# Optimization experiments

Measured on AMD Instinct MI355X. Metric: run time of the kernel, lower is better.

Reference implementation:

```python
import jax, jax.numpy as jnp
import numpy as np

N = 1_500_000
CB, CT, CO, B = 96, 128, 96, 8
BN_EPS = 1e-5


def setup_inputs() -> dict:
    key = jax.random.key(0)
    k1, k2, k3, k4 = jax.random.split(key, 4)
    return {
        "backbone_F": jax.random.normal(k1, (N, CB), dtype=jnp.float32),
        "batch_idx": jax.random.randint(k2, (N,), 0, B, dtype=jnp.int32),
        "text_feats": jax.random.normal(k3, (B, CT), dtype=jnp.float32),
        "W": jax.random.normal(k4, (CB + CT, CO), dtype=jnp.float32) * (1.0 / np.sqrt(CB + CT)),
        "gamma": jnp.ones((CO,), dtype=jnp.float32),
        "beta": jnp.zeros((CO,), dtype=jnp.float32),
    }


def reference(backbone_F, batch_idx, text_feats, W, gamma, beta):
    # gather text feats per point via batch index: [N, CT]
    rep_text = text_feats[batch_idx]
    # concat backbone + text feats: [N, CB+CT]
    combined = jnp.concatenate([backbone_F, rep_text], axis=1)
    # 1x1 sparse conv == pointwise GEMM (no bias): [N, CO]
    x = combined @ W
    # BatchNorm (training mode: batch stats over the N points)
    mean = jnp.mean(x, axis=0)
    var = jnp.var(x, axis=0)
    x = (x - mean) * jax.lax.rsqrt(var + BN_EPS) * gamma + beta
    # ReLU
    return jnp.maximum(x, 0.0)
```

## Files before the change

kernel.cpp:

```cpp
#include <hip/hip_runtime.h>
#include <hip/hip_bf16.h>

#define N_PTS 1500000
#define CBCH 96
#define CTCH 128
#define COCH 96
#define NB 8
#define BN_EPS 1e-5f

#define GSUM_OFF 0
#define GSQ_OFF 96
#define SCALE_OFF 192
#define BIAS_OFF 288
#define T_OFF 384

typedef __attribute__((ext_vector_type(8))) short bf16x8;
typedef __attribute__((ext_vector_type(4))) float f32x4;

__device__ __forceinline__ unsigned short f2bf_rne(float f) {
    union { float f; unsigned u; } v; v.f = f;
    unsigned u = v.u;
    return (unsigned short)((u + 0x7FFFu + ((u >> 16) & 1u)) >> 16);
}

__global__ void k0_init(const float* __restrict__ text, const float* __restrict__ W,
                        float* __restrict__ ws) {
    if (blockIdx.x == NB) {
        for (int i = threadIdx.x; i < 192; i += blockDim.x) ws[i] = 0.f;
        return;
    }
    int b = blockIdx.x;
    int c = threadIdx.x;
    if (c < COCH) {
        float acc = 0.f;
        #pragma unroll 8
        for (int k = 0; k < CTCH; ++k)
            acc += text[b * CTCH + k] * W[(CBCH + k) * COCH + c];
        ws[T_OFF + b * COCH + c] = acc;
    }
}

__global__ void k2_finalize(const float* __restrict__ gamma, const float* __restrict__ beta,
                            float* __restrict__ ws) {
    int c = threadIdx.x;
    if (c < COCH) {
        float mean = ws[GSUM_OFF + c] * (1.f / (float)N_PTS);
        float var  = ws[GSQ_OFF + c] * (1.f / (float)N_PTS) - mean * mean;
        float scl  = gamma[c] * rsqrtf(var + BN_EPS);
        ws[SCALE_OFF + c] = scl;
        ws[BIAS_OFF + c]  = beta[c] - mean * scl;
    }
}


__device__ __forceinline__ void load_bfrag(const float* __restrict__ W, int grp, int lr,
                                           bf16x8 bf[6][3]) {
    #pragma unroll
    for (int ct = 0; ct < 6; ++ct)
        #pragma unroll
        for (int kt = 0; kt < 3; ++kt)
            #pragma unroll
            for (int j = 0; j < 8; ++j)
                bf[ct][kt][j] = (short)f2bf_rne(W[(kt * 32 + grp * 8 + j) * COCH + ct * 16 + lr]);
}

__device__ __forceinline__ void tile_gemm(const float* __restrict__ bb,
                                          const int* __restrict__ bidx,
                                          const float* __restrict__ sT,
                                          int base, int grp, int lr,
                                          const bf16x8 bf[6][3], f32x4 acc[6]) {
    #pragma unroll
    for (int r = 0; r < 4; ++r) {
        int b = bidx[base + grp * 4 + r];
        #pragma unroll
        for (int ct = 0; ct < 6; ++ct)
            acc[ct][r] = sT[b * COCH + ct * 16 + lr];
    }
    bf16x8 af[3];
    #pragma unroll
    for (int kt = 0; kt < 3; ++kt) {
        const float4* p = reinterpret_cast<const float4*>(bb + (size_t)(base + lr) * CBCH + kt * 32 + grp * 8);
        float4 x0 = p[0], x1 = p[1];
        af[kt][0] = (short)f2bf_rne(x0.x); af[kt][1] = (short)f2bf_rne(x0.y);
        af[kt][2] = (short)f2bf_rne(x0.z); af[kt][3] = (short)f2bf_rne(x0.w);
        af[kt][4] = (short)f2bf_rne(x1.x); af[kt][5] = (short)f2bf_rne(x1.y);
        af[kt][6] = (short)f2bf_rne(x1.z); af[kt][7] = (short)f2bf_rne(x1.w);
    }
    #pragma unroll
    for (int ct = 0; ct < 6; ++ct)
        #pragma unroll
        for (int kt = 0; kt < 3; ++kt)
            acc[ct] = __builtin_amdgcn_mfma_f32_16x16x32_bf16(af[kt], bf[ct][kt], acc[ct], 0, 0, 0);
}

__global__ __launch_bounds__(256, 2) void k1_stats(const float* __restrict__ bb,
                                                   const int* __restrict__ bidx,
                                                   const float* __restrict__ W,
                                                   float* __restrict__ ws) {
    __shared__ float sT[NB * COCH];
    __shared__ float sred[2][4][COCH];
    for (int i = threadIdx.x; i < NB * COCH; i += blockDim.x) sT[i] = ws[T_OFF + i];
    __syncthreads();

    const int lane = threadIdx.x & 63;
    const int wv = threadIdx.x >> 6;
    const int grp = lane >> 4, lr = lane & 15;

    bf16x8 bf[6][3];
    load_bfrag(W, grp, lr, bf);

    float sum[6] = {0.f, 0.f, 0.f, 0.f, 0.f, 0.f};
    float sq[6] = {0.f, 0.f, 0.f, 0.f, 0.f, 0.f};

    const int gw = blockIdx.x * 4 + wv;
    const int nw = gridDim.x * 4;
    const int NT = N_PTS / 16;
    for (int t = gw; t < NT; t += nw) {
        int base = t * 16;
        f32x4 acc[6];
        tile_gemm(bb, bidx, sT, base, grp, lr, bf, acc);
        #pragma unroll
        for (int ct = 0; ct < 6; ++ct)
            #pragma unroll
            for (int r = 0; r < 4; ++r) {
                float x = acc[ct][r];
                sum[ct] += x;
                sq[ct] += x * x;
            }
    }

    #pragma unroll
    for (int ct = 0; ct < 6; ++ct) {
        float s = sum[ct], q = sq[ct];
        s += __shfl_xor(s, 16); q += __shfl_xor(q, 16);
        s += __shfl_xor(s, 32); q += __shfl_xor(q, 32);
        if (lane < 16) {
            sred[0][wv][ct * 16 + lane] = s;
            sred[1][wv][ct * 16 + lane] = q;
        }
    }
    __syncthreads();
    if (threadIdx.x < COCH) {
        int c = threadIdx.x;
        float s = sred[0][0][c] + sred[0][1][c] + sred[0][2][c] + sred[0][3][c];
        float q = sred[1][0][c] + sred[1][1][c] + sred[1][2][c] + sred[1][3][c];
        atomicAdd(&ws[GSUM_OFF + c], s);
        atomicAdd(&ws[GSQ_OFF + c], q);
    }
}

__global__ __launch_bounds__(256, 2) void k3_out(const float* __restrict__ bb,
                                                 const int* __restrict__ bidx,
                                                 const float* __restrict__ W,
                                                 const float* __restrict__ ws,
                                                 float* __restrict__ out) {
    __shared__ float sT[NB * COCH];
    for (int i = threadIdx.x; i < NB * COCH; i += blockDim.x) sT[i] = ws[T_OFF + i];
    __syncthreads();

    const int lane = threadIdx.x & 63;
    const int wv = threadIdx.x >> 6;
    const int grp = lane >> 4, lr = lane & 15;

    bf16x8 bf[6][3];
    load_bfrag(W, grp, lr, bf);

    float sc[6], bs[6];
    #pragma unroll
    for (int ct = 0; ct < 6; ++ct) {
        sc[ct] = ws[SCALE_OFF + ct * 16 + lr];
        bs[ct] = ws[BIAS_OFF + ct * 16 + lr];
    }

    const int gw = blockIdx.x * 4 + wv;
    const int nw = gridDim.x * 4;
    const int NT = N_PTS / 16;
    for (int t = gw; t < NT; t += nw) {
        int base = t * 16;
        f32x4 acc[6];
        tile_gemm(bb, bidx, sT, base, grp, lr, bf, acc);
        #pragma unroll
        for (int ct = 0; ct < 6; ++ct)
            #pragma unroll
            for (int r = 0; r < 4; ++r) {
                float y = fmaxf(acc[ct][r] * sc[ct] + bs[ct], 0.f);
                out[(size_t)(base + grp * 4 + r) * COCH + ct * 16 + lr] = y;
            }
    }
}

extern "C" void kernel_launch(void* const* d_in, const int* in_sizes, int n_in,
                              void* d_out, int out_size, void* d_ws, size_t ws_size,
                              hipStream_t stream) {
    const float* bb    = (const float*)d_in[0];
    const int*   bidx  = (const int*)d_in[1];
    const float* text  = (const float*)d_in[2];
    const float* W     = (const float*)d_in[3];
    const float* gamma = (const float*)d_in[4];
    const float* beta  = (const float*)d_in[5];
    float* out = (float*)d_out;
    float* ws  = (float*)d_ws;

    hipLaunchKernelGGL(k0_init, dim3(NB + 1), dim3(128), 0, stream, text, W, ws);
    hipLaunchKernelGGL(k1_stats, dim3(2048), dim3(256), 0, stream, bb, bidx, W, ws);
    hipLaunchKernelGGL(k2_finalize, dim3(1), dim3(128), 0, stream, gamma, beta, ws);
    hipLaunchKernelGGL(k3_out, dim3(2048), dim3(256), 0, stream, bb, bidx, W, ws, out);
}
```

Before: 377.3 us.

## Transpose output MFMA for vectorized stores, fold finalize into output kernel, reverse traversal

Swaps the MFMA operand order in the output kernel so that each lane holds four consecutive channels of one point. This lets results go out as 16-byte nontemporal vector stores instead of scattered scalar stores. The BN finalize kernel is removed and its scale/bias computation moves into the output kernel's prologue via shared memory, saving one launch. The output kernel also walks tiles in reverse order to reuse the backbone data the stats pass left in L2/cache, and loads it with nontemporal hints.

```diff
diff --git a/kernel.cpp b/kernel.cpp
--- a/kernel.cpp
+++ b/kernel.cpp
@@ -10,8 +10,6 @@
 
 #define GSUM_OFF 0
 #define GSQ_OFF 96
-#define SCALE_OFF 192
-#define BIAS_OFF 288
 #define T_OFF 384
 
 typedef __attribute__((ext_vector_type(8))) short bf16x8;
@@ -40,18 +38,6 @@
     }
 }
 
-__global__ void k2_finalize(const float* __restrict__ gamma, const float* __restrict__ beta,
-                            float* __restrict__ ws) {
-    int c = threadIdx.x;
-    if (c < COCH) {
-        float mean = ws[GSUM_OFF + c] * (1.f / (float)N_PTS);
-        float var  = ws[GSQ_OFF + c] * (1.f / (float)N_PTS) - mean * mean;
-        float scl  = gamma[c] * rsqrtf(var + BN_EPS);
-        ws[SCALE_OFF + c] = scl;
-        ws[BIAS_OFF + c]  = beta[c] - mean * scl;
-    }
-}
-
 
 __device__ __forceinline__ void load_bfrag(const float* __restrict__ W, int grp, int lr,
                                            bf16x8 bf[6][3]) {
@@ -62,35 +48,6 @@
             #pragma unroll
             for (int j = 0; j < 8; ++j)
                 bf[ct][kt][j] = (short)f2bf_rne(W[(kt * 32 + grp * 8 + j) * COCH + ct * 16 + lr]);
-}
-
-__device__ __forceinline__ void tile_gemm(const float* __restrict__ bb,
-                                          const int* __restrict__ bidx,
-                                          const float* __restrict__ sT,
-                                          int base, int grp, int lr,
-                                          const bf16x8 bf[6][3], f32x4 acc[6]) {
-    #pragma unroll
-    for (int r = 0; r < 4; ++r) {
-        int b = bidx[base + grp * 4 + r];
-        #pragma unroll
-        for (int ct = 0; ct < 6; ++ct)
-            acc[ct][r] = sT[b * COCH + ct * 16 + lr];
-    }
-    bf16x8 af[3];
-    #pragma unroll
-    for (int kt = 0; kt < 3; ++kt) {
-        const float4* p = reinterpret_cast<const float4*>(bb + (size_t)(base + lr) * CBCH + kt * 32 + grp * 8);
-        float4 x0 = p[0], x1 = p[1];
-        af[kt][0] = (short)f2bf_rne(x0.x); af[kt][1] = (short)f2bf_rne(x0.y);
-        af[kt][2] = (short)f2bf_rne(x0.z); af[kt][3] = (short)f2bf_rne(x0.w);
-        af[kt][4] = (short)f2bf_rne(x1.x); af[kt][5] = (short)f2bf_rne(x1.y);
-        af[kt][6] = (short)f2bf_rne(x1.z); af[kt][7] = (short)f2bf_rne(x1.w);
-    }
-    #pragma unroll
-    for (int ct = 0; ct < 6; ++ct)
-        #pragma unroll
-        for (int kt = 0; kt < 3; ++kt)
-            acc[ct] = __builtin_amdgcn_mfma_f32_16x16x32_bf16(af[kt], bf[ct][kt], acc[ct], 0, 0, 0);
 }
 
 __global__ __launch_bounds__(256, 2) void k1_stats(const float* __restrict__ bb,
@@ -118,7 +75,29 @@
     for (int t = gw; t < NT; t += nw) {
         int base = t * 16;
         f32x4 acc[6];
-        tile_gemm(bb, bidx, sT, base, grp, lr, bf, acc);
+        #pragma unroll
+        for (int r = 0; r < 4; ++r) {
+            int b = bidx[base + grp * 4 + r];
+            #pragma unroll
+            for (int ct = 0; ct < 6; ++ct)
+                acc[ct][r] = sT[b * COCH + ct * 16 + lr];
+        }
+        bf16x8 af[3];
+        #pragma unroll
+        for (int kt = 0; kt < 3; ++kt) {
+            const f32x4* p = reinterpret_cast<const f32x4*>(bb + (size_t)(base + lr) * CBCH + kt * 32 + grp * 8);
+            f32x4 x0 = p[0], x1 = p[1];
+            #pragma unroll
+            for (int j = 0; j < 4; ++j) {
+                af[kt][j]     = (short)f2bf_rne(x0[j]);
+                af[kt][4 + j] = (short)f2bf_rne(x1[j]);
+            }
+        }
+        #pragma unroll
+        for (int ct = 0; ct < 6; ++ct)
+            #pragma unroll
+            for (int kt = 0; kt < 3; ++kt)
+                acc[ct] = __builtin_amdgcn_mfma_f32_16x16x32_bf16(af[kt], bf[ct][kt], acc[ct], 0, 0, 0);
         #pragma unroll
         for (int ct = 0; ct < 6; ++ct)
             #pragma unroll
@@ -152,10 +131,22 @@
 __global__ __launch_bounds__(256, 2) void k3_out(const float* __restrict__ bb,
                                                  const int* __restrict__ bidx,
                                                  const float* __restrict__ W,
+                                                 const float* __restrict__ gamma,
+                                                 const float* __restrict__ beta,
                                                  const float* __restrict__ ws,
                                                  float* __restrict__ out) {
     __shared__ float sT[NB * COCH];
+    __shared__ float sScale[COCH];
+    __shared__ float sBias[COCH];
     for (int i = threadIdx.x; i < NB * COCH; i += blockDim.x) sT[i] = ws[T_OFF + i];
+    if (threadIdx.x < COCH) {
+        int c = threadIdx.x;
+        float mean = ws[GSUM_OFF + c] * (1.f / (float)N_PTS);
+        float var  = ws[GSQ_OFF + c] * (1.f / (float)N_PTS) - mean * mean;
+        float scl  = gamma[c] * rsqrtf(var + BN_EPS);
+        sScale[c] = scl;
+        sBias[c]  = beta[c] - mean * scl;
+    }
     __syncthreads();
 
     const int lane = threadIdx.x & 63;
@@ -165,27 +156,51 @@
     bf16x8 bf[6][3];
     load_bfrag(W, grp, lr, bf);
 
-    float sc[6], bs[6];
+    f32x4 sc[6], bs[6];
     #pragma unroll
     for (int ct = 0; ct < 6; ++ct) {
-        sc[ct] = ws[SCALE_OFF + ct * 16 + lr];
-        bs[ct] = ws[BIAS_OFF + ct * 16 + lr];
+        sc[ct] = *reinterpret_cast<const f32x4*>(&sScale[ct * 16 + grp * 4]);
+        bs[ct] = *reinterpret_cast<const f32x4*>(&sBias[ct * 16 + grp * 4]);
     }
 
     const int gw = blockIdx.x * 4 + wv;
     const int nw = gridDim.x * 4;
     const int NT = N_PTS / 16;
-    for (int t = gw; t < NT; t += nw) {
+    for (int t = NT - 1 - gw; t >= 0; t -= nw) {
         int base = t * 16;
+        int b = bidx[base + lr];
         f32x4 acc[6];
-        tile_gemm(bb, bidx, sT, base, grp, lr, bf, acc);
-        #pragma unroll
-        for (int ct = 0; ct < 6; ++ct)
-            #pragma unroll
-            for (int r = 0; r < 4; ++r) {
-                float y = fmaxf(acc[ct][r] * sc[ct] + bs[ct], 0.f);
-                out[(size_t)(base + grp * 4 + r) * COCH + ct * 16 + lr] = y;
+        #pragma unroll
+        for (int ct = 0; ct < 6; ++ct)
+            acc[ct] = *reinterpret_cast<const f32x4*>(&sT[b * COCH + ct * 16 + grp * 4]);
+
+        bf16x8 pf[3];
+        #pragma unroll
+        for (int kt = 0; kt < 3; ++kt) {
+            const f32x4* p = reinterpret_cast<const f32x4*>(bb + (size_t)(base + lr) * CBCH + kt * 32 + grp * 8);
+            f32x4 x0 = __builtin_nontemporal_load(p);
+            f32x4 x1 = __builtin_nontemporal_load(p + 1);
+            #pragma unroll
+            for (int j = 0; j < 4; ++j) {
+                pf[kt][j]     = (short)f2bf_rne(x0[j]);
+                pf[kt][4 + j] = (short)f2bf_rne(x1[j]);
             }
+        }
+        #pragma unroll
+        for (int ct = 0; ct < 6; ++ct)
+            #pragma unroll
+            for (int kt = 0; kt < 3; ++kt)
+                acc[ct] = __builtin_amdgcn_mfma_f32_16x16x32_bf16(bf[ct][kt], pf[kt], acc[ct], 0, 0, 0);
+
+        #pragma unroll
+        for (int ct = 0; ct < 6; ++ct) {
+            f32x4 y;
+            #pragma unroll
+            for (int r = 0; r < 4; ++r)
+                y[r] = fmaxf(acc[ct][r] * sc[ct][r] + bs[ct][r], 0.f);
+            __builtin_nontemporal_store(y,
+                reinterpret_cast<f32x4*>(out + (size_t)(base + lr) * COCH + ct * 16 + grp * 4));
+        }
     }
 }
 
@@ -203,6 +218,5 @@
 
     hipLaunchKernelGGL(k0_init, dim3(NB + 1), dim3(128), 0, stream, text, W, ws);
     hipLaunchKernelGGL(k1_stats, dim3(2048), dim3(256), 0, stream, bb, bidx, W, ws);
-    hipLaunchKernelGGL(k2_finalize, dim3(1), dim3(128), 0, stream, gamma, beta, ws);
-    hipLaunchKernelGGL(k3_out, dim3(2048), dim3(256), 0, stream, bb, bidx, W, ws, out);
-}
+    hipLaunchKernelGGL(k3_out, dim3(2048), dim3(256), 0, stream, bb, bidx, W, gamma, beta, ws, out);
+}
```

After: 376.4 us. Within noise of the previous version (-0.2%).
